# Kernel optimization log

Hardware: AMD Instinct MI355X
Metric: run time of the kernel (lower is better)

Reference implementation:

```python
import jax, jax.numpy as jnp
import numpy as np

B, S, D, E, H = 4, 2048, 1024, 8, 2048


def setup_inputs() -> dict:
    key = jax.random.key(0)
    ks = jax.random.split(key, 8)
    s_in = 1.0 / np.sqrt(D)   # torch Linear default init scale (uniform bound)
    s_hid = 1.0 / np.sqrt(H)
    return {
        "x": jax.random.normal(ks[0], (B, S, D), dtype=jnp.float32),
        "W1": jax.random.uniform(ks[1], (E, D, H), minval=-s_in, maxval=s_in, dtype=jnp.float32),
        "b1": jax.random.uniform(ks[2], (E, H), minval=-s_in, maxval=s_in, dtype=jnp.float32),
        "W2": jax.random.uniform(ks[3], (E, H, D), minval=-s_hid, maxval=s_hid, dtype=jnp.float32),
        "b2": jax.random.uniform(ks[4], (E, D), minval=-s_hid, maxval=s_hid, dtype=jnp.float32),
        "Wg": jax.random.uniform(ks[5], (D, E), minval=-s_in, maxval=s_in, dtype=jnp.float32),
        "bg": jax.random.uniform(ks[6], (E,), minval=-s_in, maxval=s_in, dtype=jnp.float32),
    }


def reference(x, W1, b1, W2, b2, Wg, bg):
    # All-experts dense MoE (eval mode: dropout is identity).
    # hidden: [B,S,E,H]
    h = jax.nn.relu(jnp.einsum("bsd,edh->bseh", x, W1) + b1)
    # expert outputs: [B,S,E,D]
    expert_out = jnp.einsum("bseh,ehd->bsed", h, W2) + b2
    # gate (raw linear, no softmax in original): [B,S,E]
    gate = jnp.einsum("bsd,de->bse", x, Wg) + bg
    # gate-weighted sum over experts -> [B,S,D]
    return jnp.einsum("bse,bsed->bsd", gate, expert_out)
```

## Files before the change

kernel.cpp:

```cpp
#include <hip/hip_runtime.h>

#define NTOK 8192
#define DDIM 1024
#define HDIM 2048
#define NEXP 8
#define GEXP 2

#define BM 256
#define BN 128
#define BK 64

typedef unsigned short u16;
typedef short bf16x8 __attribute__((ext_vector_type(8)));
typedef float f32x4 __attribute__((ext_vector_type(4)));
typedef float float4_t __attribute__((ext_vector_type(4)));

__device__ __forceinline__ u16 f2bf(float f) {
  unsigned u = __float_as_uint(f);
  u += 0x7FFFu + ((u >> 16) & 1u);
  return (u16)(u >> 16);
}

#define GLOAD_LDS16(gp, lp)                                                     \
  __builtin_amdgcn_global_load_lds(                                             \
      (const __attribute__((address_space(1))) unsigned int*)(gp),              \
      (__attribute__((address_space(3))) unsigned int*)(lp), 16, 0, 0)

__global__ void k_prep(const float* __restrict__ x, const float* __restrict__ Wg,
                       const float* __restrict__ bg,
                       u16* __restrict__ xb, float* __restrict__ gate) {
  const int tok = (blockIdx.x * 256 + threadIdx.x) >> 6;
  const int lane = threadIdx.x & 63;
  const float* xr = x + (size_t)tok * DDIM;
  u16* xo = xb + (size_t)tok * DDIM;
  float s[NEXP];
#pragma unroll
  for (int e = 0; e < NEXP; ++e) s[e] = 0.f;
#pragma unroll
  for (int it = 0; it < 2; ++it) {
    const int d0 = lane * 8 + it * 512;
    float4_t v0 = *(const float4_t*)(xr + d0);
    float4_t v1 = *(const float4_t*)(xr + d0 + 4);
    union { bf16x8 v; u16 h[8]; } u;
    u.h[0] = f2bf(v0.x); u.h[1] = f2bf(v0.y); u.h[2] = f2bf(v0.z); u.h[3] = f2bf(v0.w);
    u.h[4] = f2bf(v1.x); u.h[5] = f2bf(v1.y); u.h[6] = f2bf(v1.z); u.h[7] = f2bf(v1.w);
    *(bf16x8*)(xo + d0) = u.v;
    float xv[8] = {v0.x, v0.y, v0.z, v0.w, v1.x, v1.y, v1.z, v1.w};
#pragma unroll
    for (int j = 0; j < 8; ++j) {
      const float4_t w0 = *(const float4_t*)(Wg + (size_t)(d0 + j) * NEXP);
      const float4_t w1 = *(const float4_t*)(Wg + (size_t)(d0 + j) * NEXP + 4);
      s[0] += xv[j] * w0.x; s[1] += xv[j] * w0.y;
      s[2] += xv[j] * w0.z; s[3] += xv[j] * w0.w;
      s[4] += xv[j] * w1.x; s[5] += xv[j] * w1.y;
      s[6] += xv[j] * w1.z; s[7] += xv[j] * w1.w;
    }
  }
#pragma unroll
  for (int off = 32; off; off >>= 1)
#pragma unroll
    for (int e = 0; e < NEXP; ++e) s[e] += __shfl_down(s[e], off);
  if (lane == 0) {
#pragma unroll
    for (int e = 0; e < NEXP; ++e) gate[(size_t)tok * NEXP + e] = s[e] + bg[e];
  }
}

__global__ void k_transpose(const float* __restrict__ in, u16* __restrict__ out,
                            int R, int C, size_t oexp, int orstride) {
  __shared__ float t[64][65];
  const int rb = blockIdx.x * 64, cb = blockIdx.y * 64;
  const float* pin = in + (size_t)blockIdx.z * R * C;
  u16* pout = out + (size_t)blockIdx.z * oexp;
  const int tid = threadIdx.x;
  {
    const int r = tid >> 4;
    const int c4 = (tid & 15) * 4;
#pragma unroll
    for (int i = 0; i < 4; ++i) {
      float4_t v = *(const float4_t*)(pin + (size_t)(rb + r + 16 * i) * C + cb + c4);
      t[r + 16 * i][c4 + 0] = v.x;
      t[r + 16 * i][c4 + 1] = v.y;
      t[r + 16 * i][c4 + 2] = v.z;
      t[r + 16 * i][c4 + 3] = v.w;
    }
  }
  __syncthreads();
  {
    const int oc = tid >> 3;
    const int r8 = (tid & 7) * 8;
#pragma unroll
    for (int jp = 0; jp < 2; ++jp) {
      const int ocol = oc + 32 * jp;
      union { bf16x8 v; u16 h[8]; } u;
#pragma unroll
      for (int k = 0; k < 8; ++k) u.h[k] = f2bf(t[r8 + k][ocol]);
      *(bf16x8*)(pout + (size_t)(cb + ocol) * orstride + rb + r8) = u.v;
    }
  }
}

template <int MODE, int BCH>
__global__ __launch_bounds__(512, 2) void k_gemm(
    const u16* __restrict__ A, int lda,
    const u16* __restrict__ Bt, int ldb,
    const float* __restrict__ bias,
    const float* __restrict__ gate, int ebase,
    void* __restrict__ Cout, int ldc,
    int tilesN, int K, int accum, int ca, int cb) {
  __shared__ __align__(16) u16 lds[3 * (BM + BN) * BK];
  const int tid = threadIdx.x;
  const int lane = tid & 63;
  const int wid = tid >> 6;
  const int wm = wid >> 1;
  const int wn = wid & 1;

  int wg = blockIdx.x;
  int xcd = wg & 7, lo = wg >> 3;
  int cgcols = tilesN / cb;
  int cr = xcd / cgcols, cc = xcd % cgcols;
  int tm = cr * ca + lo / cb;
  int tn = cc * cb + lo % cb;
  int bm = tm * BM, bn = tn * BN;

  const int srow = tid >> 3;
  const int scol = ((tid & 7) ^ (srow & 7)) << 3;
  const u16* gA = A + (size_t)(bm + srow) * lda + scol;
  const u16* gB = Bt + (size_t)(bn + srow) * ldb + scol;
  const int dofs = wid * 512;

  u16* a0 = lds;            u16* b0 = lds + BM * BK;
  u16* a1 = b0 + BN * BK;   u16* b1p = a1 + BM * BK;
  u16* a2 = b1p + BN * BK;  u16* b2p = a2 + BM * BK;

#define BOFF(kt) (BCH ? ((size_t)((kt) >> 5) * ((size_t)DDIM * HDIM) +          \
                         (size_t)((kt) & 31) * BK)                              \
                      : (size_t)(kt) * BK)

#define STAGE(aD, bD, kt)                                                       \
  {                                                                             \
    const u16* sa_ = gA + (size_t)(kt) * BK;                                    \
    const u16* sb_ = gB + BOFF(kt);                                             \
    GLOAD_LDS16(sa_,                       (aD) + dofs);                        \
    GLOAD_LDS16(sa_ + (size_t)64 * lda,    (aD) + 4096 + dofs);                 \
    GLOAD_LDS16(sa_ + (size_t)128 * lda,   (aD) + 8192 + dofs);                 \
    GLOAD_LDS16(sa_ + (size_t)192 * lda,   (aD) + 12288 + dofs);                \
    GLOAD_LDS16(sb_,                       (bD) + dofs);                        \
    GLOAD_LDS16(sb_ + (size_t)64 * ldb,    (bD) + 4096 + dofs);                 \
  }

  const int fr = lane & 15;
  const int fq = lane >> 4;
  const int xr = fr & 7;
  const int so0 = ((0 + fq) ^ xr) << 3;
  const int so1 = ((4 + fq) ^ xr) << 3;
  int aro[4], bro[4];
#pragma unroll
  for (int m = 0; m < 4; ++m) aro[m] = (wm * 64 + m * 16 + fr) << 6;
#pragma unroll
  for (int n = 0; n < 4; ++n) bro[n] = (wn * 64 + n * 16 + fr) << 6;

  f32x4 acc[4][4] = {};
  const int nkt = K >> 6;

  STAGE(a0, b0, 0);
  STAGE(a1, b1p, 1);
  asm volatile("s_waitcnt vmcnt(6)" ::: "memory");
  __builtin_amdgcn_s_barrier();
  __builtin_amdgcn_sched_barrier(0);

  u16 *aC = a0, *bC = b0, *aN = a1, *bN = b1p, *aF = a2, *bF = b2p;

#pragma unroll 1
  for (int t = 0; t < nkt; ++t) {
    if (t + 2 < nkt) STAGE(aF, bF, t + 2);
#pragma unroll
    for (int kk = 0; kk < 2; ++kk) {
      const int so = kk ? so1 : so0;
      bf16x8 af[4], bfv[4];
#pragma unroll
      for (int m = 0; m < 4; ++m) af[m] = *(const bf16x8*)(aC + aro[m] + so);
#pragma unroll
      for (int n = 0; n < 4; ++n) bfv[n] = *(const bf16x8*)(bC + bro[n] + so);
      __builtin_amdgcn_s_setprio(1);
#pragma unroll
      for (int m = 0; m < 4; ++m)
#pragma unroll
        for (int n = 0; n < 4; ++n)
          acc[m][n] = __builtin_amdgcn_mfma_f32_16x16x32_bf16(af[m], bfv[n],
                                                              acc[m][n], 0, 0, 0);
      __builtin_amdgcn_s_setprio(0);
    }
    if (t != nkt - 1) {
      if (t + 2 < nkt) {
        asm volatile("s_waitcnt vmcnt(6)" ::: "memory");
      } else {
        asm volatile("s_waitcnt vmcnt(0)" ::: "memory");
      }
      __builtin_amdgcn_s_barrier();
      __builtin_amdgcn_sched_barrier(0);
      u16* tp;
      tp = aC; aC = aN; aN = aF; aF = tp;
      tp = bC; bC = bN; bN = bF; bF = tp;
    }
  }

  const int colbase = bn + wn * 64 + fr;
  if (MODE == 1) {
    const int e = ebase + ((bn + wn * 64) >> 11);
    float bcol[4];
#pragma unroll
    for (int n = 0; n < 4; ++n) bcol[n] = bias[colbase + n * 16];
    u16* O = (u16*)Cout;
#pragma unroll
    for (int m = 0; m < 4; ++m) {
#pragma unroll
      for (int j = 0; j < 4; ++j) {
        int r = bm + wm * 64 + m * 16 + fq * 4 + j;
        float g = gate[(size_t)r * NEXP + e];
#pragma unroll
        for (int n = 0; n < 4; ++n) {
          float v = fmaxf(acc[m][n][j] + bcol[n], 0.f) * g;
          O[(size_t)r * ldc + colbase + n * 16] = f2bf(v);
        }
      }
    }
  } else {
    float* O = (float*)Cout;
    float b2c[4][NEXP];
    if (!accum) {
#pragma unroll
      for (int n = 0; n < 4; ++n)
#pragma unroll
        for (int e = 0; e < NEXP; ++e)
          b2c[n][e] = bias[(size_t)e * DDIM + colbase + n * 16];
    }
#pragma unroll
    for (int m = 0; m < 4; ++m) {
#pragma unroll
      for (int j = 0; j < 4; ++j) {
        int r = bm + wm * 64 + m * 16 + fq * 4 + j;
        if (!accum) {
          float g8[NEXP];
#pragma unroll
          for (int e = 0; e < NEXP; ++e) g8[e] = gate[(size_t)r * NEXP + e];
#pragma unroll
          for (int n = 0; n < 4; ++n) {
            float v = acc[m][n][j];
#pragma unroll
            for (int e = 0; e < NEXP; ++e) v += g8[e] * b2c[n][e];
            O[(size_t)r * DDIM + colbase + n * 16] = v;
          }
        } else {
#pragma unroll
          for (int n = 0; n < 4; ++n) {
            size_t idx = (size_t)r * DDIM + colbase + n * 16;
            O[idx] += acc[m][n][j];
          }
        }
      }
    }
  }
#undef STAGE
#undef BOFF
}

extern "C" void kernel_launch(void* const* d_in, const int* in_sizes, int n_in,
                              void* d_out, int out_size, void* d_ws, size_t ws_size,
                              hipStream_t stream) {
  (void)in_sizes; (void)n_in; (void)out_size;
  const float* x  = (const float*)d_in[0];
  const float* W1 = (const float*)d_in[1];
  const float* b1 = (const float*)d_in[2];
  const float* W2 = (const float*)d_in[3];
  const float* b2 = (const float*)d_in[4];
  const float* Wg = (const float*)d_in[5];
  const float* bg = (const float*)d_in[6];
  float* out = (float*)d_out;

  size_t o_xb   = 0;
  size_t o_w1t  = o_xb  + (size_t)NTOK * DDIM * 2;
  size_t o_w2t  = o_w1t + (size_t)NEXP * HDIM * DDIM * 2;
  size_t o_gate = o_w2t + (size_t)NEXP * DDIM * HDIM * 2;
  size_t o_h    = o_gate + (size_t)NTOK * NEXP * 4;
  size_t need   = o_h   + (size_t)NTOK * GEXP * HDIM * 2;
  if (ws_size < need) return;

  u16*   xb   = (u16*)((char*)d_ws + o_xb);
  u16*   W1t  = (u16*)((char*)d_ws + o_w1t);
  u16*   W2t  = (u16*)((char*)d_ws + o_w2t);
  float* gate = (float*)((char*)d_ws + o_gate);
  u16*   hbuf = (u16*)((char*)d_ws + o_h);

  k_prep<<<NTOK / 4, 256, 0, stream>>>(x, Wg, bg, xb, gate);
  dim3 g1(DDIM / 64, HDIM / 64, NEXP);
  k_transpose<<<g1, 256, 0, stream>>>(W1, W1t, DDIM, HDIM, (size_t)HDIM * DDIM, DDIM);
  dim3 g2(HDIM / 64, DDIM / 64, NEXP);
  k_transpose<<<g2, 256, 0, stream>>>(W2, W2t, HDIM, DDIM, (size_t)DDIM * HDIM, HDIM);

  const int Ng = GEXP * HDIM;
  for (int g = 0; g < NEXP / GEXP; ++g) {
    k_gemm<1, 0><<<(NTOK / BM) * (Ng / BN), 512, 0, stream>>>(
        xb, DDIM, W1t + (size_t)g * Ng * DDIM, DDIM,
        b1 + (size_t)g * Ng, gate, g * GEXP,
        hbuf, Ng, Ng / BN, DDIM, 0, 16, 8);
    k_gemm<2, 1><<<(NTOK / BM) * (DDIM / BN), 512, 0, stream>>>(
        hbuf, Ng, W2t + (size_t)g * GEXP * DDIM * HDIM, HDIM,
        b2, gate, 0,
        out, DDIM, DDIM / BN, Ng, g > 0, 8, 4);
  }
}
```

Baseline: 690.0 us.

## Restructure GEMM into 8-wave 256-wide tiles with quadrant-phased load/compute interleave

The bf16 MFMA GEMM moves from 256x128 tiles with triple buffering to 256x256 tiles (GEMM1) and 128x256 tiles (GEMM2), split across 8 waves in a 2x4 layout and double-buffered. Each K step runs as four quadrant phases, and global-to-LDS loads for the next stages are issued between phases, with barriers in between. The aim is more data reuse per tile and finer overlap of memory traffic with MFMA work. The costs are more barriers per K step, fewer workgroups (512 and 256) and higher register pressure.

```diff
diff --git a/kernel.cpp b/kernel.cpp
--- a/kernel.cpp
+++ b/kernel.cpp
@@ -5,10 +5,6 @@
 #define HDIM 2048
 #define NEXP 8
 #define GEXP 2
-
-#define BM 256
-#define BN 128
-#define BK 64
 
 typedef unsigned short u16;
 typedef short bf16x8 __attribute__((ext_vector_type(8)));
@@ -100,20 +96,24 @@
   }
 }
 
-template <int MODE, int BCH>
-__global__ __launch_bounds__(512, 2) void k_gemm(
+template <int MODE, int BCH, int TBM>
+__global__ __launch_bounds__(512, 2) void k_gemm8(
     const u16* __restrict__ A, int lda,
     const u16* __restrict__ Bt, int ldb,
     const float* __restrict__ bias,
     const float* __restrict__ gate, int ebase,
     void* __restrict__ Cout, int ldc,
     int tilesN, int K, int accum, int ca, int cb) {
-  __shared__ __align__(16) u16 lds[3 * (BM + BN) * BK];
+  constexpr int MREPH = TBM / 64;
+  constexpr int AH = TBM / 128;
+  __shared__ __align__(16) u16 lds[2 * (TBM + 256) * 64];
   const int tid = threadIdx.x;
   const int lane = tid & 63;
   const int wid = tid >> 6;
-  const int wm = wid >> 1;
-  const int wn = wid & 1;
+  const int wm = wid >> 2;
+  const int wn = wid & 3;
+  const int wmr = wm * (TBM / 4);
+  const int wnr = wn * 32;
 
   int wg = blockIdx.x;
   int xcd = wg & 7, lo = wg >> 3;
@@ -121,7 +121,7 @@
   int cr = xcd / cgcols, cc = xcd % cgcols;
   int tm = cr * ca + lo / cb;
   int tn = cc * cb + lo % cb;
-  int bm = tm * BM, bn = tn * BN;
+  int bm = tm * TBM, bn = tn * 256;
 
   const int srow = tid >> 3;
   const int scol = ((tid & 7) ^ (srow & 7)) << 3;
@@ -129,139 +129,165 @@
   const u16* gB = Bt + (size_t)(bn + srow) * ldb + scol;
   const int dofs = wid * 512;
 
-  u16* a0 = lds;            u16* b0 = lds + BM * BK;
-  u16* a1 = b0 + BN * BK;   u16* b1p = a1 + BM * BK;
-  u16* a2 = b1p + BN * BK;  u16* b2p = a2 + BM * BK;
+  u16* aB0 = lds;
+  u16* bB0 = lds + TBM * 64;
+  u16* aB1 = lds + (TBM + 256) * 64;
+  u16* bB1 = aB1 + TBM * 64;
 
 #define BOFF(kt) (BCH ? ((size_t)((kt) >> 5) * ((size_t)DDIM * HDIM) +          \
-                         (size_t)((kt) & 31) * BK)                              \
-                      : (size_t)(kt) * BK)
-
-#define STAGE(aD, bD, kt)                                                       \
-  {                                                                             \
-    const u16* sa_ = gA + (size_t)(kt) * BK;                                    \
-    const u16* sb_ = gB + BOFF(kt);                                             \
-    GLOAD_LDS16(sa_,                       (aD) + dofs);                        \
-    GLOAD_LDS16(sa_ + (size_t)64 * lda,    (aD) + 4096 + dofs);                 \
-    GLOAD_LDS16(sa_ + (size_t)128 * lda,   (aD) + 8192 + dofs);                 \
-    GLOAD_LDS16(sa_ + (size_t)192 * lda,   (aD) + 12288 + dofs);                \
-    GLOAD_LDS16(sb_,                       (bD) + dofs);                        \
-    GLOAD_LDS16(sb_ + (size_t)64 * ldb,    (bD) + 4096 + dofs);                 \
-  }
+                         (size_t)((kt) & 31) * 64)                              \
+                      : (size_t)(kt) * 64)
+#define STG_A(dst, hh, ts)                                                      \
+  { _Pragma("unroll") for (int j_ = 0; j_ < AH; ++j_)                           \
+      GLOAD_LDS16(gA + (size_t)((hh) * (TBM / 2) + j_ * 64) * lda +             \
+                      (size_t)(ts) * 64,                                        \
+                  (dst) + ((hh) * (TBM / 2) + j_ * 64) * 64 + dofs); }
+#define STG_B(dst, hh, ts)                                                      \
+  { _Pragma("unroll") for (int j_ = 0; j_ < 2; ++j_)                            \
+      GLOAD_LDS16(gB + (size_t)((hh) * 128 + j_ * 64) * ldb + BOFF(ts),         \
+                  (dst) + ((hh) * 128 + j_ * 64) * 64 + dofs); }
+#define VMC_N()                                                                 \
+  { if (TBM == 256) asm volatile("s_waitcnt vmcnt(4)" ::: "memory");            \
+    else            asm volatile("s_waitcnt vmcnt(3)" ::: "memory"); }
 
   const int fr = lane & 15;
   const int fq = lane >> 4;
   const int xr = fr & 7;
   const int so0 = ((0 + fq) ^ xr) << 3;
   const int so1 = ((4 + fq) ^ xr) << 3;
-  int aro[4], bro[4];
-#pragma unroll
-  for (int m = 0; m < 4; ++m) aro[m] = (wm * 64 + m * 16 + fr) << 6;
-#pragma unroll
-  for (int n = 0; n < 4; ++n) bro[n] = (wn * 64 + n * 16 + fr) << 6;
-
-  f32x4 acc[4][4] = {};
+
+  f32x4 acc[4][MREPH][2] = {};
+
+#define QPHASE(MH, NH, aCur, bCur)                                              \
+  {                                                                             \
+    bf16x8 av[MREPH][2], bv[2][2];                                              \
+    _Pragma("unroll") for (int i_ = 0; i_ < MREPH; ++i_) {                      \
+      const int rb_ = ((MH) * (TBM / 2) + wmr + i_ * 16 + fr) << 6;             \
+      av[i_][0] = *(const bf16x8*)((aCur) + rb_ + so0);                         \
+      av[i_][1] = *(const bf16x8*)((aCur) + rb_ + so1);                         \
+    }                                                                           \
+    _Pragma("unroll") for (int n_ = 0; n_ < 2; ++n_) {                          \
+      const int rb_ = ((NH) * 128 + wnr + n_ * 16 + fr) << 6;                   \
+      bv[n_][0] = *(const bf16x8*)((bCur) + rb_ + so0);                         \
+      bv[n_][1] = *(const bf16x8*)((bCur) + rb_ + so1);                         \
+    }                                                                           \
+    __builtin_amdgcn_s_barrier();                                               \
+    asm volatile("s_waitcnt lgkmcnt(0)" ::: "memory");                          \
+    __builtin_amdgcn_sched_barrier(0);                                          \
+    __builtin_amdgcn_s_setprio(1);                                              \
+    _Pragma("unroll") for (int i_ = 0; i_ < MREPH; ++i_)                        \
+      _Pragma("unroll") for (int n_ = 0; n_ < 2; ++n_) {                        \
+        acc[(MH) * 2 + (NH)][i_][n_] = __builtin_amdgcn_mfma_f32_16x16x32_bf16( \
+            av[i_][0], bv[n_][0], acc[(MH) * 2 + (NH)][i_][n_], 0, 0, 0);       \
+        acc[(MH) * 2 + (NH)][i_][n_] = __builtin_amdgcn_mfma_f32_16x16x32_bf16( \
+            av[i_][1], bv[n_][1], acc[(MH) * 2 + (NH)][i_][n_], 0, 0, 0);       \
+      }                                                                         \
+    __builtin_amdgcn_s_setprio(0);                                              \
+  }
+
   const int nkt = K >> 6;
 
-  STAGE(a0, b0, 0);
-  STAGE(a1, b1p, 1);
-  asm volatile("s_waitcnt vmcnt(6)" ::: "memory");
+  STG_A(aB0, 0, 0); STG_B(bB0, 0, 0); STG_A(aB0, 1, 0); STG_B(bB0, 1, 0);
+  STG_A(aB1, 0, 1); STG_B(bB1, 0, 1);
+  VMC_N();
   __builtin_amdgcn_s_barrier();
-  __builtin_amdgcn_sched_barrier(0);
-
-  u16 *aC = a0, *bC = b0, *aN = a1, *bN = b1p, *aF = a2, *bF = b2p;
+
+  u16 *aC_ = aB0, *bC_ = bB0, *aN_ = aB1, *bN_ = bB1;
 
 #pragma unroll 1
   for (int t = 0; t < nkt; ++t) {
-    if (t + 2 < nkt) STAGE(aF, bF, t + 2);
-#pragma unroll
-    for (int kk = 0; kk < 2; ++kk) {
-      const int so = kk ? so1 : so0;
-      bf16x8 af[4], bfv[4];
-#pragma unroll
-      for (int m = 0; m < 4; ++m) af[m] = *(const bf16x8*)(aC + aro[m] + so);
-#pragma unroll
-      for (int n = 0; n < 4; ++n) bfv[n] = *(const bf16x8*)(bC + bro[n] + so);
-      __builtin_amdgcn_s_setprio(1);
-#pragma unroll
-      for (int m = 0; m < 4; ++m)
-#pragma unroll
-        for (int n = 0; n < 4; ++n)
-          acc[m][n] = __builtin_amdgcn_mfma_f32_16x16x32_bf16(af[m], bfv[n],
-                                                              acc[m][n], 0, 0, 0);
-      __builtin_amdgcn_s_setprio(0);
-    }
-    if (t != nkt - 1) {
-      if (t + 2 < nkt) {
-        asm volatile("s_waitcnt vmcnt(6)" ::: "memory");
-      } else {
-        asm volatile("s_waitcnt vmcnt(0)" ::: "memory");
-      }
-      __builtin_amdgcn_s_barrier();
-      __builtin_amdgcn_sched_barrier(0);
-      u16* tp;
-      tp = aC; aC = aN; aN = aF; aF = tp;
-      tp = bC; bC = bN; bN = bF; bF = tp;
-    }
-  }
-
-  const int colbase = bn + wn * 64 + fr;
+    const bool s1ok = (t + 1 < nkt);
+    const bool s2ok = (t + 2 < nkt);
+    if (s1ok) STG_A(aN_, 1, t + 1);
+    QPHASE(0, 0, aC_, bC_);
+    __builtin_amdgcn_s_barrier();
+    if (s1ok) STG_B(bN_, 1, t + 1);
+    QPHASE(0, 1, aC_, bC_);
+    __builtin_amdgcn_s_barrier();
+    if (s2ok) STG_A(aC_, 0, t + 2);
+    QPHASE(1, 0, aC_, bC_);
+    __builtin_amdgcn_s_barrier();
+    if (s2ok) STG_B(bC_, 0, t + 2);
+    QPHASE(1, 1, aC_, bC_);
+    if (s2ok) { VMC_N(); }
+    else      { asm volatile("s_waitcnt vmcnt(0)" ::: "memory"); }
+    __builtin_amdgcn_s_barrier();
+    u16* tp;
+    tp = aC_; aC_ = aN_; aN_ = tp;
+    tp = bC_; bC_ = bN_; bN_ = tp;
+  }
+
   if (MODE == 1) {
-    const int e = ebase + ((bn + wn * 64) >> 11);
-    float bcol[4];
-#pragma unroll
-    for (int n = 0; n < 4; ++n) bcol[n] = bias[colbase + n * 16];
     u16* O = (u16*)Cout;
 #pragma unroll
-    for (int m = 0; m < 4; ++m) {
-#pragma unroll
-      for (int j = 0; j < 4; ++j) {
-        int r = bm + wm * 64 + m * 16 + fq * 4 + j;
-        float g = gate[(size_t)r * NEXP + e];
-#pragma unroll
-        for (int n = 0; n < 4; ++n) {
-          float v = fmaxf(acc[m][n][j] + bcol[n], 0.f) * g;
-          O[(size_t)r * ldc + colbase + n * 16] = f2bf(v);
-        }
-      }
-    }
-  } else {
-    float* O = (float*)Cout;
-    float b2c[4][NEXP];
-    if (!accum) {
-#pragma unroll
-      for (int n = 0; n < 4; ++n)
-#pragma unroll
-        for (int e = 0; e < NEXP; ++e)
-          b2c[n][e] = bias[(size_t)e * DDIM + colbase + n * 16];
-    }
-#pragma unroll
-    for (int m = 0; m < 4; ++m) {
-#pragma unroll
-      for (int j = 0; j < 4; ++j) {
-        int r = bm + wm * 64 + m * 16 + fq * 4 + j;
-        if (!accum) {
-          float g8[NEXP];
-#pragma unroll
-          for (int e = 0; e < NEXP; ++e) g8[e] = gate[(size_t)r * NEXP + e];
-#pragma unroll
-          for (int n = 0; n < 4; ++n) {
-            float v = acc[m][n][j];
-#pragma unroll
-            for (int e = 0; e < NEXP; ++e) v += g8[e] * b2c[n][e];
-            O[(size_t)r * DDIM + colbase + n * 16] = v;
-          }
-        } else {
-#pragma unroll
-          for (int n = 0; n < 4; ++n) {
-            size_t idx = (size_t)r * DDIM + colbase + n * 16;
-            O[idx] += acc[m][n][j];
+    for (int q = 0; q < 4; ++q) {
+      const int MH = q >> 1, NH = q & 1;
+      const int cb0 = bn + NH * 128 + wnr;
+      const int e = ebase + (cb0 >> 11);
+      float bcol[2];
+#pragma unroll
+      for (int n = 0; n < 2; ++n) bcol[n] = bias[cb0 + n * 16 + fr];
+#pragma unroll
+      for (int i = 0; i < MREPH; ++i) {
+#pragma unroll
+        for (int j = 0; j < 4; ++j) {
+          int r = bm + MH * (TBM / 2) + wmr + i * 16 + fq * 4 + j;
+          float g = gate[(size_t)r * NEXP + e];
+#pragma unroll
+          for (int n = 0; n < 2; ++n) {
+            float v = fmaxf(acc[q][i][n][j] + bcol[n], 0.f) * g;
+            O[(size_t)r * ldc + cb0 + n * 16 + fr] = f2bf(v);
           }
         }
       }
     }
-  }
-#undef STAGE
+  } else {
+    float* O = (float*)Cout;
+    float b2c[2][2][NEXP];
+    if (!accum) {
+#pragma unroll
+      for (int nh = 0; nh < 2; ++nh)
+#pragma unroll
+        for (int n = 0; n < 2; ++n)
+#pragma unroll
+          for (int e = 0; e < NEXP; ++e)
+            b2c[nh][n][e] = bias[(size_t)e * DDIM + bn + nh * 128 + wnr + n * 16 + fr];
+    }
+#pragma unroll
+    for (int q = 0; q < 4; ++q) {
+      const int MH = q >> 1, NH = q & 1;
+      const int cb0 = bn + NH * 128 + wnr;
+#pragma unroll
+      for (int i = 0; i < MREPH; ++i) {
+#pragma unroll
+        for (int j = 0; j < 4; ++j) {
+          int r = bm + MH * (TBM / 2) + wmr + i * 16 + fq * 4 + j;
+          if (!accum) {
+            float g8[NEXP];
+#pragma unroll
+            for (int e = 0; e < NEXP; ++e) g8[e] = gate[(size_t)r * NEXP + e];
+#pragma unroll
+            for (int n = 0; n < 2; ++n) {
+              float v = acc[q][i][n][j];
+#pragma unroll
+              for (int e = 0; e < NEXP; ++e) v += g8[e] * b2c[NH][n][e];
+              O[(size_t)r * DDIM + cb0 + n * 16 + fr] = v;
+            }
+          } else {
+#pragma unroll
+            for (int n = 0; n < 2; ++n) {
+              size_t idx = (size_t)r * DDIM + cb0 + n * 16 + fr;
+              O[idx] += acc[q][i][n][j];
+            }
+          }
+        }
+      }
+    }
+  }
+#undef QPHASE
+#undef STG_A
+#undef STG_B
+#undef VMC_N
 #undef BOFF
 }
 
@@ -300,13 +326,13 @@
 
   const int Ng = GEXP * HDIM;
   for (int g = 0; g < NEXP / GEXP; ++g) {
-    k_gemm<1, 0><<<(NTOK / BM) * (Ng / BN), 512, 0, stream>>>(
+    k_gemm8<1, 0, 256><<<512, 512, 0, stream>>>(
         xb, DDIM, W1t + (size_t)g * Ng * DDIM, DDIM,
         b1 + (size_t)g * Ng, gate, g * GEXP,
-        hbuf, Ng, Ng / BN, DDIM, 0, 16, 8);
-    k_gemm<2, 1><<<(NTOK / BM) * (DDIM / BN), 512, 0, stream>>>(
+        hbuf, Ng, Ng / 256, DDIM, 0, 8, 8);
+    k_gemm8<2, 1, 128><<<256, 512, 0, stream>>>(
         hbuf, Ng, W2t + (size_t)g * GEXP * DDIM * HDIM, HDIM,
         b2, gate, 0,
-        out, DDIM, DDIM / BN, Ng, g > 0, 8, 4);
-  }
-}
+        out, DDIM, DDIM / 256, Ng, g > 0, 8, 4);
+  }
+}
```

Result: slower. 767.1 us (+11.2%).
